# Performance work log

Hardware: AMD Instinct MI355X
Metric: run time of the kernel (lower is better)

Reference implementation:

```python
import jax, jax.numpy as jnp
import numpy as np

D = 512          # latent_dim
H = 8            # num_heads
NLAYERS = 8
DFF = 8          # fast_transformers d_ff slot receives num_heads in the repo (kept faithful)
NC = 10          # NUM_CLUSTERS
KMEANS_ITERS = 10
NJ, NF, T, BS = 25, 6, 1024, 16
NCLS, MAXA = 12, 6


def _pe(S, d):
    pos = jnp.arange(S, dtype=jnp.float32)[:, None]
    div = jnp.exp(jnp.arange(0, d, 2, dtype=jnp.float32) * (-np.log(10000.0) / d))
    pe = jnp.zeros((S, d), jnp.float32)
    pe = pe.at[:, 0::2].set(jnp.sin(pos * div))
    pe = pe.at[:, 1::2].set(jnp.cos(pos * div))
    return pe


def _ln(x, g, b, eps=1e-5):
    m = jnp.mean(x, -1, keepdims=True)
    v = jnp.var(x, -1, keepdims=True)
    return (x - m) * jax.lax.rsqrt(v + eps) * g + b


def _clustered_attn_one(q, k, v):
    # q, k, v: (L, Dh). Cluster queries (Lloyd k-means, deterministic init from
    # first NC queries), attend with centroids, broadcast back to queries.
    cent = q[:NC]
    for _ in range(KMEANS_ITERS):
        d = jnp.sum(cent * cent, -1)[None, :] - 2.0 * (q @ cent.T)  # (L, C)
        a = jnp.argmin(d, -1)
        oh = jax.nn.one_hot(a, NC, dtype=q.dtype)                   # (L, C)
        cent = (oh.T @ q) / jnp.maximum(oh.sum(0), 1.0)[:, None]
    d = jnp.sum(cent * cent, -1)[None, :] - 2.0 * (q @ cent.T)
    a = jnp.argmin(d, -1)                                           # (L,)
    temp = 1.0 / np.sqrt(q.shape[-1])
    A = jax.nn.softmax((cent @ k.T) * temp, -1)                     # (C, L)
    return (A @ v)[a]                                               # (L, Dh)


def _layer(z, Wq, bq, Wk, bk, Wv, bv, Wo, bo, g1, c1, g2, c2, W1, b1, W2, b2):
    B, S, d = z.shape
    Dh = d // H
    q = (z @ Wq + bq).reshape(B, S, H, Dh).transpose(0, 2, 1, 3).reshape(B * H, S, Dh)
    k = (z @ Wk + bk).reshape(B, S, H, Dh).transpose(0, 2, 1, 3).reshape(B * H, S, Dh)
    v = (z @ Wv + bv).reshape(B, S, H, Dh).transpose(0, 2, 1, 3).reshape(B * H, S, Dh)
    o = jax.vmap(_clustered_attn_one)(q, k, v)
    o = o.reshape(B, H, S, Dh).transpose(0, 2, 1, 3).reshape(B, S, d)
    z = z + (o @ Wo + bo)                     # post-norm TransformerEncoderLayer
    z = _ln(z, g1, c1)
    y = jax.nn.relu(z @ W1 + b1) @ W2 + b2    # d_ff == num_heads (repo bug, kept)
    return _ln(z + y, g2, c2)


def _forward(x, muQuery, sigmaQuery, mu_w, mu_b, sig_w, sig_b, skel_w, skel_b,
             Wq, bq, Wk, bk, Wv, bv, Wo, bo, g1, c1, g2, c2, W1, b1, W2, b2, y):
    bs, nj, nf, nframes = x.shape
    h = x.transpose(3, 0, 1, 2).reshape(nframes, bs, nj * nf) @ skel_w + skel_b  # (T,B,D)
    mu_enc = muQuery[y].reshape(bs, -1) @ mu_w + mu_b          # (B, D)
    sig_enc = sigmaQuery[y].reshape(bs, -1) @ sig_w + sig_b    # (B, D)
    xseq = jnp.concatenate([mu_enc[None], sig_enc[None], h], 0)  # (S, B, D)
    S = xseq.shape[0]
    xseq = xseq + _pe(S, xseq.shape[-1])[:, None, :]
    z = xseq.transpose(1, 0, 2)  # (B, S, D): attend over the sequence axis
    for i in range(NLAYERS):
        z = _layer(z, Wq[i], bq[i], Wk[i], bk[i], Wv[i], bv[i], Wo[i], bo[i],
                   g1[i], c1[i], g2[i], c2[i], W1[i], b1[i], W2[i], b2[i])
    out = z.transpose(1, 0, 2)  # (S, B, D)
    return out[0], out[1]       # mu, logvar: (B, D) each


def setup_inputs() -> dict:
    key = jax.random.key(0)
    ks = jax.random.split(key, 20)
    s = 0.02
    return {
        "x": jax.random.normal(ks[0], (BS, NJ, NF, T), jnp.float32),
        "y": jax.random.randint(ks[1], (BS, MAXA), 0, NCLS),
        "mask": jnp.ones((BS, T), bool),
        "muQuery": jax.random.normal(ks[2], (NCLS, D), jnp.float32),
        "sigmaQuery": jax.random.normal(ks[3], (NCLS + 1, D), jnp.float32),
        "mu_w": jax.random.normal(ks[4], (D * MAXA, D), jnp.float32) * s,
        "mu_b": jnp.zeros((D,), jnp.float32),
        "sig_w": jax.random.normal(ks[5], (D * MAXA, D), jnp.float32) * s,
        "sig_b": jnp.zeros((D,), jnp.float32),
        "skel_w": jax.random.normal(ks[6], (NJ * NF, D), jnp.float32) * s,
        "skel_b": jnp.zeros((D,), jnp.float32),
        "Wq": jax.random.normal(ks[7], (NLAYERS, D, D), jnp.float32) * s,
        "bq": jnp.zeros((NLAYERS, D), jnp.float32),
        "Wk": jax.random.normal(ks[8], (NLAYERS, D, D), jnp.float32) * s,
        "bk": jnp.zeros((NLAYERS, D), jnp.float32),
        "Wv": jax.random.normal(ks[9], (NLAYERS, D, D), jnp.float32) * s,
        "bv": jnp.zeros((NLAYERS, D), jnp.float32),
        "Wo": jax.random.normal(ks[10], (NLAYERS, D, D), jnp.float32) * s,
        "bo": jnp.zeros((NLAYERS, D), jnp.float32),
        "g1": jnp.ones((NLAYERS, D), jnp.float32),
        "c1": jnp.zeros((NLAYERS, D), jnp.float32),
        "g2": jnp.ones((NLAYERS, D), jnp.float32),
        "c2": jnp.zeros((NLAYERS, D), jnp.float32),
        "W1": jax.random.normal(ks[11], (NLAYERS, D, DFF), jnp.float32) * s,
        "b1": jnp.zeros((NLAYERS, DFF), jnp.float32),
        "W2": jax.random.normal(ks[12], (NLAYERS, DFF, D), jnp.float32) * s,
        "b2": jnp.zeros((NLAYERS, D), jnp.float32),
    }


def reference(x, y, mask, muQuery, sigmaQuery, mu_w, mu_b, sig_w, sig_b,
              skel_w, skel_b, Wq, bq, Wk, bk, Wv, bv, Wo, bo,
              g1, c1, g2, c2, W1, b1, W2, b2):
    del mask  # computed but never passed to the encoder in the original code
    mu, logvar = _forward(x, muQuery, sigmaQuery, mu_w, mu_b, sig_w, sig_b,
                          skel_w, skel_b, Wq, bq, Wk, bk, Wv, bv, Wo, bo,
                          g1, c1, g2, c2, W1, b1, W2, b2, y)
    return mu, logvar
```

## Files before the change

kernel.cpp:

```cpp
#include <hip/hip_runtime.h>
#include <hip/hip_fp16.h>
#include <math.h>

#define D 512
#define H 8
#define DH 64
#define NLAYERS 8
#define DFF 8
#define NC 10
#define KITERS 10
#define SEQ 1026
#define SEQP 1032
#define BATCH 16
#define MR (BATCH*SEQ)
#define NBUF ((size_t)MR * D)
#define DD ((size_t)D * D)
#define NBH (BATCH*H)

typedef _Float16 f16;
typedef f16 f16x8 __attribute__((ext_vector_type(8)));
typedef float f32x4 __attribute__((ext_vector_type(4)));

__device__ __forceinline__ void split2(float x, float y, unsigned& uh, unsigned& ul) {
    __half hx = __float2half_rn(x), hy = __float2half_rn(y);
    __half lx = __float2half_rn(x - __half2float(hx));
    __half ly = __float2half_rn(y - __half2float(hy));
    uh = (unsigned)__half_as_ushort(hx) | ((unsigned)__half_as_ushort(hy) << 16);
    ul = (unsigned)__half_as_ushort(lx) | ((unsigned)__half_as_ushort(ly) << 16);
}

__device__ __forceinline__ float pe_val(int s, int d) {
    float e = (float)(d & ~1);
    float dv = expf(e * (-9.210340371976184f / 512.0f));
    float ph = (float)s * dv;
    return (d & 1) ? cosf(ph) : sinf(ph);
}

__launch_bounds__(256)
__global__ void convert_w(const float* __restrict__ Wq, const float* __restrict__ Wk,
                          const float* __restrict__ Wv,
                          ushort* __restrict__ whiT, ushort* __restrict__ wloT)
{
    __shared__ float tile[64][65];
    const int tid = threadIdx.x;
    const int k0 = blockIdx.x * 64, n0 = blockIdx.y * 64, m = blockIdx.z;
    const int which = m % 3, lyr = m / 3;
    const float* base;
    switch (which) { case 0: base = Wq; break; case 1: base = Wk; break;
                     default: base = Wv; }
    const float* W = base + (size_t)lyr * DD;
    {
        int r = tid >> 4, c = (tid & 15) * 4;
        #pragma unroll
        for (int p = 0; p < 4; ++p) {
            float4 v = *(const float4*)&W[(size_t)(k0 + r + p*16)*D + n0 + c];
            tile[r + p*16][c]   = v.x; tile[r + p*16][c+1] = v.y;
            tile[r + p*16][c+2] = v.z; tile[r + p*16][c+3] = v.w;
        }
    }
    __syncthreads();
    ushort* ohp = whiT + (size_t)m * DD;
    ushort* olp = wloT + (size_t)m * DD;
    {
        int nl = tid >> 3, kc = (tid & 7) * 8;
        #pragma unroll
        for (int p = 0; p < 2; ++p) {
            int n = nl + p*32;
            uint4 UH, UL;
            split2(tile[kc+0][n], tile[kc+1][n], UH.x, UL.x);
            split2(tile[kc+2][n], tile[kc+3][n], UH.y, UL.y);
            split2(tile[kc+4][n], tile[kc+5][n], UH.z, UL.z);
            split2(tile[kc+6][n], tile[kc+7][n], UH.w, UL.w);
            size_t off = (size_t)(n0 + n)*D + k0 + kc;
            *(uint4*)&ohp[off] = UH;
            *(uint4*)&olp[off] = UL;
        }
    }
}

__launch_bounds__(256)
__global__ void embed_kernel(const float* __restrict__ x, const int* __restrict__ y,
    const float* __restrict__ muQ, const float* __restrict__ sigQ,
    const float* __restrict__ mu_w, const float* __restrict__ mu_b,
    const float* __restrict__ sig_w, const float* __restrict__ sig_b,
    const float* __restrict__ skel_w, const float* __restrict__ skel_b,
    float* __restrict__ z)
{
    __shared__ float xin[3072];
    const int bx = blockIdx.x, b = blockIdx.y, tid = threadIdx.x;
    if (bx < 2) {
        const float* Q  = (bx == 0) ? muQ  : sigQ;
        const float* W  = (bx == 0) ? mu_w : sig_w;
        const float* bb = (bx == 0) ? mu_b : sig_b;
        for (int i = tid; i < 3072; i += 256) {
            int a = y[b*6 + (i >> 9)];
            xin[i] = Q[a*D + (i & 511)];
        }
        __syncthreads();
        const int d0 = tid, d1 = tid + 256;
        float acc0 = bb[d0], acc1 = bb[d1];
        const float4* x4 = (const float4*)xin;
        for (int i4 = 0; i4 < 768; ++i4) {
            float4 xv = x4[i4];
            int r = i4 * 4;
            acc0 += xv.x*W[(size_t)(r+0)*D+d0] + xv.y*W[(size_t)(r+1)*D+d0]
                  + xv.z*W[(size_t)(r+2)*D+d0] + xv.w*W[(size_t)(r+3)*D+d0];
            acc1 += xv.x*W[(size_t)(r+0)*D+d1] + xv.y*W[(size_t)(r+1)*D+d1]
                  + xv.z*W[(size_t)(r+2)*D+d1] + xv.w*W[(size_t)(r+3)*D+d1];
        }
        size_t base = ((size_t)b*SEQ + bx) * D;
        z[base + d0] = acc0 + pe_val(bx, d0);
        z[base + d1] = acc1 + pe_val(bx, d1);
    } else {
        const int f0 = (bx - 2) * 4;
        for (int idx = tid; idx < 600; idx += 256) {
            int i = idx >> 2, ff = idx & 3;
            xin[idx] = x[((size_t)(b*150 + i))*1024 + f0 + ff];
        }
        __syncthreads();
        const float4* x4 = (const float4*)xin;
        for (int dd = 0; dd < 2; ++dd) {
            const int d = tid + dd*256;
            float a0, a1, a2, a3;
            a0 = a1 = a2 = a3 = skel_b[d];
            for (int i = 0; i < 150; ++i) {
                float4 xv = x4[i];
                float w = skel_w[(size_t)i*D + d];
                a0 += xv.x*w; a1 += xv.y*w; a2 += xv.z*w; a3 += xv.w*w;
            }
            float a[4] = {a0, a1, a2, a3};
            #pragma unroll
            for (int ff = 0; ff < 4; ++ff) {
                int s = f0 + ff + 2;
                z[((size_t)b*SEQ + s)*D + d] = a[ff] + pe_val(s, d);
            }
        }
    }
}

__launch_bounds__(256)
__global__ void gemm_qkv(const float* __restrict__ A,
                         const ushort* __restrict__ Bhi_b, const ushort* __restrict__ Blo_b,
                         const float* __restrict__ bq, const float* __restrict__ bk,
                         const float* __restrict__ bv,
                         float* __restrict__ outbase, int M)
{
    __shared__ ushort Ah[128*40], Al[128*40], Bh[128*40], Bl[128*40];
    const int tid = threadIdx.x;
    const int m0 = blockIdx.y * 128, n0 = blockIdx.x * 128;
    const int zz = blockIdx.z;
    const ushort* Bhi = Bhi_b + (size_t)zz * DD;
    const ushort* Blo = Blo_b + (size_t)zz * DD;
    const float* bias = (zz == 0) ? bq : (zz == 1) ? bk : bv;
    float* out = outbase + (size_t)zz * NBUF;
    const int l = tid & 63, wv = tid >> 6;
    const int wr = wv >> 1, wc = wv & 1;

    f32x4 acc[4][4];
    #pragma unroll
    for (int mi = 0; mi < 4; ++mi)
        #pragma unroll
        for (int ni = 0; ni < 4; ++ni) acc[mi][ni] = (f32x4){0.f, 0.f, 0.f, 0.f};

    const int ar_s = tid >> 1, ac_s = (tid & 1) * 16;
    const bool va = (m0 + ar_s) < M;
    const int r0 = (tid*2) >> 2,   kc0 = ((tid*2) & 3) * 8;
    const int r1 = (tid*2+1) >> 2, kc1 = ((tid*2+1) & 3) * 8;
    const float4 fz = make_float4(0.f, 0.f, 0.f, 0.f);

    for (int kt = 0; kt < 16; ++kt) {
        const int kb = kt * 32;
        float4 a0 = fz, a1 = fz, a2 = fz, a3 = fz;
        if (va) {
            const float4* ap = (const float4*)&A[(size_t)(m0 + ar_s)*D + kb + ac_s];
            a0 = ap[0]; a1 = ap[1]; a2 = ap[2]; a3 = ap[3];
        }
        uint4 bh0 = *(const uint4*)&Bhi[(size_t)(n0+r0)*D + kb + kc0];
        uint4 bh1 = *(const uint4*)&Bhi[(size_t)(n0+r1)*D + kb + kc1];
        uint4 bl0 = *(const uint4*)&Blo[(size_t)(n0+r0)*D + kb + kc0];
        uint4 bl1 = *(const uint4*)&Blo[(size_t)(n0+r1)*D + kb + kc1];

        uint4 AH0, AL0, AH1, AL1;
        split2(a0.x, a0.y, AH0.x, AL0.x); split2(a0.z, a0.w, AH0.y, AL0.y);
        split2(a1.x, a1.y, AH0.z, AL0.z); split2(a1.z, a1.w, AH0.w, AL0.w);
        split2(a2.x, a2.y, AH1.x, AL1.x); split2(a2.z, a2.w, AH1.y, AL1.y);
        split2(a3.x, a3.y, AH1.z, AL1.z); split2(a3.z, a3.w, AH1.w, AL1.w);

        if (kt) __syncthreads();
        *(uint4*)&Ah[ar_s*40 + ac_s]     = AH0;
        *(uint4*)&Ah[ar_s*40 + ac_s + 8] = AH1;
        *(uint4*)&Al[ar_s*40 + ac_s]     = AL0;
        *(uint4*)&Al[ar_s*40 + ac_s + 8] = AL1;
        *(uint4*)&Bh[r0*40 + kc0] = bh0;  *(uint4*)&Bh[r1*40 + kc1] = bh1;
        *(uint4*)&Bl[r0*40 + kc0] = bl0;  *(uint4*)&Bl[r1*40 + kc1] = bl1;
        __syncthreads();

        const int ko = (l >> 4) * 8;
        f16x8 bhf[4], blf[4];
        #pragma unroll
        for (int ni = 0; ni < 4; ++ni) {
            int br = wc*64 + ni*16 + (l & 15);
            bhf[ni] = *(const f16x8*)&Bh[br*40 + ko];
            blf[ni] = *(const f16x8*)&Bl[br*40 + ko];
        }
        #pragma unroll
        for (int mi = 0; mi < 4; ++mi) {
            int ar = wr*64 + mi*16 + (l & 15);
            f16x8 ahf = *(const f16x8*)&Ah[ar*40 + ko];
            f16x8 alf = *(const f16x8*)&Al[ar*40 + ko];
            #pragma unroll
            for (int ni = 0; ni < 4; ++ni) {
                acc[mi][ni] = __builtin_amdgcn_mfma_f32_16x16x32_f16(ahf, bhf[ni], acc[mi][ni], 0, 0, 0);
                acc[mi][ni] = __builtin_amdgcn_mfma_f32_16x16x32_f16(ahf, blf[ni], acc[mi][ni], 0, 0, 0);
                acc[mi][ni] = __builtin_amdgcn_mfma_f32_16x16x32_f16(alf, bhf[ni], acc[mi][ni], 0, 0, 0);
            }
        }
    }

    const int col_base = n0 + wc*64 + (l & 15);
    const int row_base = m0 + wr*64 + ((l >> 4) << 2);
    #pragma unroll
    for (int ni = 0; ni < 4; ++ni) {
        const int col = col_base + ni*16;
        const float bv2 = bias[col];
        #pragma unroll
        for (int mi = 0; mi < 4; ++mi) {
            #pragma unroll
            for (int e = 0; e < 4; ++e) {
                const int row = row_base + mi*16 + e;
                if (row >= M) continue;
                float val = acc[mi][ni][e] + bv2;
                int bb = row / SEQ;
                int ss = row - bb*SEQ;
                int hh = col >> 6, dh = col & 63;
                out[((size_t)(bb*H + hh)*SEQ + ss)*DH + dh] = val;
            }
        }
    }
}

__launch_bounds__(1024, 4)
__global__ void attn_kernel(const float* __restrict__ q, const float* __restrict__ kk,
                            const float* __restrict__ v,
                            float* __restrict__ centout, unsigned char* __restrict__ assignout)
{
    __shared__ float At[NC][SEQP];
    __shared__ float cent[NC][DH];
    __shared__ float tailrow[2][DH];
    __shared__ float cnorm[NC];
    __shared__ int   cnt[NC];
    __shared__ int   chg;
    __shared__ unsigned char assign[1028];
    __shared__ float redA[16][NC];
    __shared__ float redB[16][NC];
    __shared__ float Mc[NC];
    __shared__ float Sinv[NC];

    const int tid = threadIdx.x;
    const int wv = tid >> 6, lane = tid & 63;
    const int bh = blockIdx.x;
    const float* qh = q  + (size_t)bh * SEQ * DH;
    const float* kh = kk + (size_t)bh * SEQ * DH;
    const float* vh = v  + (size_t)bh * SEQ * DH;
    float* part = &At[0][0];

    if (tid < NC*DH) ((float*)cent)[tid] = qh[tid];
    if (tid >= NC*DH && tid < NC*DH + 2*DH) ((float*)tailrow)[tid - NC*DH] = qh[1024*DH + (tid - NC*DH)];
    __syncthreads();

    const float4* qrow4 = (const float4*)(qh + (size_t)tid * DH);
    int prev_a = -1, prev_t = -1;

    for (int iter = 0; iter <= KITERS; ++iter) {
        if (tid < NC) {
            float sn = 0.f;
            #pragma unroll
            for (int i = 0; i < 16; ++i) {
                float4 cv = *(const float4*)&cent[tid][i*4];
                sn += cv.x*cv.x + cv.y*cv.y + cv.z*cv.z + cv.w*cv.w;
            }
            cnorm[tid] = sn;
            cnt[tid] = 0;
        }
        if (tid == 0) chg = 0;
        __syncthreads();

        int a_reg;
        {
            float acc[NC];
            #pragma unroll
            for (int c = 0; c < NC; ++c) acc[c] = 0.f;
            #pragma unroll 8
            for (int kq = 0; kq < 16; ++kq) {
                float4 qv = qrow4[kq];
                #pragma unroll
                for (int c = 0; c < NC; ++c) {
                    float4 cv = *(const float4*)&cent[c][kq*4];
                    acc[c] += qv.x*cv.x + qv.y*cv.y + qv.z*cv.z + qv.w*cv.w;
                }
            }
            int best = 0; float bd = 1e30f;
            #pragma unroll
            for (int c = 0; c < NC; ++c) {
                float dd = cnorm[c] - 2.f*acc[c];
                if (dd < bd) { bd = dd; best = c; }
            }
            a_reg = best;
            assign[tid] = (unsigned char)best;
        }
        {
            unsigned long long mm = __ballot(a_reg != prev_a);
            if (lane == 0 && mm) atomicAdd(&chg, 1);
            prev_a = a_reg;
        }
        if (iter < KITERS) {
            #pragma unroll
            for (int c = 0; c < NC; ++c) {
                unsigned long long m = __ballot(a_reg == c);
                if (lane == 0 && m) atomicAdd(&cnt[c], __popcll(m));
            }
        }
        if (tid < 2) {
            int best = 0; float bd = 1e30f;
            #pragma unroll
            for (int c = 0; c < NC; ++c) {
                float acc = 0.f;
                #pragma unroll
                for (int i = 0; i < 64; ++i) acc += tailrow[tid][i]*cent[c][i];
                float dd = cnorm[c] - 2.f*acc;
                if (dd < bd) { bd = dd; best = c; }
            }
            assign[1024 + tid] = (unsigned char)best;
            if (best != prev_t) atomicAdd(&chg, 1);
            prev_t = best;
            if (iter < KITERS) atomicAdd(&cnt[best], 1);
        }
        __syncthreads();
        if (iter == KITERS) break;
        if (chg == 0) break;

        {
            float accq[NC];
            #pragma unroll
            for (int c = 0; c < NC; ++c) accq[c] = 0.f;
            const int s0 = wv * 64;
            #pragma unroll 8
            for (int i = 0; i < 64; ++i) {
                int s = s0 + i;
                float qv = qh[(size_t)s*DH + lane];
                int c = assign[s];
                #pragma unroll
                for (int cc = 0; cc < NC; ++cc) accq[cc] += (cc == c) ? qv : 0.f;
            }
            if (wv < 2) {
                int c = assign[1024 + wv];
                float qv = tailrow[wv][lane];
                #pragma unroll
                for (int cc = 0; cc < NC; ++cc) accq[cc] += (cc == c) ? qv : 0.f;
            }
            #pragma unroll
            for (int c = 0; c < NC; ++c) part[(wv*NC + c)*DH + lane] = accq[c];
        }
        __syncthreads();
        if (tid < NC*DH) {
            int c = tid >> 6;
            float s = 0.f;
            #pragma unroll
            for (int w = 0; w < 16; ++w) s += part[w*(NC*DH) + tid];
            ((float*)cent)[tid] = s / fmaxf((float)cnt[c], 1.f);
        }
        __syncthreads();
    }

    if (tid < 2*DH) ((float*)tailrow)[tid] = kh[1024*DH + tid];
    __syncthreads();

    float lg[NC], lgt[NC];
    {
        const float4* krow4 = (const float4*)(kh + (size_t)tid * DH);
        #pragma unroll
        for (int c = 0; c < NC; ++c) lg[c] = 0.f;
        #pragma unroll 8
        for (int kq = 0; kq < 16; ++kq) {
            float4 kv = krow4[kq];
            #pragma unroll
            for (int c = 0; c < NC; ++c) {
                float4 cv = *(const float4*)&cent[c][kq*4];
                lg[c] += kv.x*cv.x + kv.y*cv.y + kv.z*cv.z + kv.w*cv.w;
            }
        }
        #pragma unroll
        for (int c = 0; c < NC; ++c) lg[c] *= 0.125f;
    }
    if (tid < 2) {
        #pragma unroll
        for (int c = 0; c < NC; ++c) {
            float acc = 0.f;
            #pragma unroll
            for (int i = 0; i < 64; ++i) acc += tailrow[tid][i]*cent[c][i];
            lgt[c] = 0.125f * acc;
        }
    }

    #pragma unroll
    for (int c = 0; c < NC; ++c) {
        float m = lg[c];
        if (tid < 2) m = fmaxf(m, lgt[c]);
        #pragma unroll
        for (int off = 32; off; off >>= 1) m = fmaxf(m, __shfl_xor(m, off, 64));
        if (lane == 0) redA[wv][c] = m;
    }
    __syncthreads();
    if (tid < NC) {
        float m = redA[0][tid];
        #pragma unroll
        for (int w = 1; w < 16; ++w) m = fmaxf(m, redA[w][tid]);
        Mc[tid] = m;
    }
    __syncthreads();
    #pragma unroll
    for (int c = 0; c < NC; ++c) lg[c] = expf(lg[c] - Mc[c]);
    if (tid < 2) {
        #pragma unroll
        for (int c = 0; c < NC; ++c) lgt[c] = expf(lgt[c] - Mc[c]);
    }
    #pragma unroll
    for (int c = 0; c < NC; ++c) {
        float s = lg[c] + ((tid < 2) ? lgt[c] : 0.f);
        #pragma unroll
        for (int off = 32; off; off >>= 1) s += __shfl_xor(s, off, 64);
        if (lane == 0) redB[wv][c] = s;
    }
    __syncthreads();
    if (tid < NC) {
        float s = 0.f;
        #pragma unroll
        for (int w = 0; w < 16; ++w) s += redB[w][tid];
        Sinv[tid] = 1.f / s;
    }
    __syncthreads();
    #pragma unroll
    for (int c = 0; c < NC; ++c) At[c][tid] = lg[c] * Sinv[c];
    if (tid < 2) {
        #pragma unroll
        for (int c = 0; c < NC; ++c) At[c][1024 + tid] = lgt[c] * Sinv[c];
    }
    __syncthreads();

    {
        float accv[NC];
        #pragma unroll
        for (int c = 0; c < NC; ++c) accv[c] = 0.f;
        const int s0 = wv * 64;
        for (int i = 0; i < 64; i += 4) {
            float vv0 = vh[(size_t)(s0+i  )*DH + lane];
            float vv1 = vh[(size_t)(s0+i+1)*DH + lane];
            float vv2 = vh[(size_t)(s0+i+2)*DH + lane];
            float vv3 = vh[(size_t)(s0+i+3)*DH + lane];
            #pragma unroll
            for (int c = 0; c < NC; ++c) {
                float4 av = *(const float4*)&At[c][s0+i];
                accv[c] += av.x*vv0 + av.y*vv1 + av.z*vv2 + av.w*vv3;
            }
        }
        if (wv < 2) {
            int s = 1024 + wv;
            float vv = vh[(size_t)s*DH + lane];
            #pragma unroll
            for (int c = 0; c < NC; ++c) accv[c] += At[c][s] * vv;
        }
        __syncthreads();
        #pragma unroll
        for (int c = 0; c < NC; ++c) part[(wv*NC + c)*DH + lane] = accv[c];
    }
    __syncthreads();
    if (tid < NC*DH) {
        float s = 0.f;
        #pragma unroll
        for (int w = 0; w < 16; ++w) s += part[w*(NC*DH) + tid];
        centout[(size_t)bh*(NC*DH) + tid] = s;
    }
    for (int i = tid; i < SEQ; i += 1024)
        assignout[(size_t)bh*SEQP + i] = assign[i];
}

__launch_bounds__(256)
__global__ void pproj_kernel(const float* __restrict__ centout, const float* __restrict__ Wo,
                             float* __restrict__ P)
{
    __shared__ float cs[NC][DH];
    const int tid = threadIdx.x;
    const int bh = blockIdx.x, h = bh & 7;
    const int n = blockIdx.y * 256 + tid;
    for (int i = tid; i < NC*DH; i += 256) ((float*)cs)[i] = centout[(size_t)bh*(NC*DH) + i];
    __syncthreads();
    float acc[NC];
    #pragma unroll
    for (int c = 0; c < NC; ++c) acc[c] = 0.f;
    #pragma unroll 8
    for (int d = 0; d < DH; ++d) {
        float wv = Wo[(size_t)(h*DH + d)*D + n];
        #pragma unroll
        for (int c = 0; c < NC; ++c) acc[c] += cs[c][d] * wv;
    }
    #pragma unroll
    for (int c = 0; c < NC; ++c)
        P[((size_t)bh*NC + c)*D + n] = acc[c];
}

__launch_bounds__(256)
__global__ void ffn_ln_kernel(float* __restrict__ z,
    const float* __restrict__ P, const unsigned char* __restrict__ assignbuf,
    const float* __restrict__ bo,
    const float* __restrict__ g1, const float* __restrict__ c1,
    const float* __restrict__ W1, const float* __restrict__ b1,
    const float* __restrict__ W2, const float* __restrict__ b2,
    const float* __restrict__ g2, const float* __restrict__ c2)
{
    __shared__ float red[8];
    __shared__ float redh[4][DFF];
    const int row = blockIdx.x, tid = threadIdx.x;
    const int lane = tid & 63, wid = tid >> 6;
    const int b = row / SEQ, s = row - b*SEQ;

    float x0 = z[(size_t)row*D + tid]       + bo[tid];
    float x1 = z[(size_t)row*D + tid + 256] + bo[tid + 256];
    #pragma unroll
    for (int h = 0; h < H; ++h) {
        int a = assignbuf[(size_t)(b*H + h)*SEQP + s];
        const float* Pr = P + ((size_t)(b*H + h)*NC + a)*D;
        x0 += Pr[tid];
        x1 += Pr[tid + 256];
    }

    float sm = x0 + x1, ss = x0*x0 + x1*x1;
    #pragma unroll
    for (int off = 32; off; off >>= 1) {
        sm += __shfl_xor(sm, off, 64);
        ss += __shfl_xor(ss, off, 64);
    }
    if (lane == 0) { red[wid] = sm; red[4 + wid] = ss; }
    __syncthreads();
    float tot  = red[0] + red[1] + red[2] + red[3];
    float tot2 = red[4] + red[5] + red[6] + red[7];
    float mean = tot * (1.f/512.f);
    float var  = tot2 * (1.f/512.f) - mean*mean;
    float rstd = rsqrtf(var + 1e-5f);
    float za = (x0 - mean)*rstd*g1[tid]       + c1[tid];
    float zb = (x1 - mean)*rstd*g1[tid + 256] + c1[tid + 256];

    float p[DFF];
    #pragma unroll
    for (int j = 0; j < DFF; ++j)
        p[j] = za * W1[(size_t)tid*DFF + j] + zb * W1[(size_t)(tid+256)*DFF + j];
    #pragma unroll
    for (int off = 32; off; off >>= 1)
        #pragma unroll
        for (int j = 0; j < DFF; ++j) p[j] += __shfl_xor(p[j], off, 64);
    if (lane == 0) {
        #pragma unroll
        for (int j = 0; j < DFF; ++j) redh[wid][j] = p[j];
    }
    __syncthreads();
    float hv[DFF];
    #pragma unroll
    for (int j = 0; j < DFF; ++j)
        hv[j] = fmaxf(redh[0][j] + redh[1][j] + redh[2][j] + redh[3][j] + b1[j], 0.f);
    float y0 = b2[tid], y1 = b2[tid + 256];
    #pragma unroll
    for (int j = 0; j < DFF; ++j) {
        y0 += hv[j] * W2[(size_t)j*D + tid];
        y1 += hv[j] * W2[(size_t)j*D + tid + 256];
    }
    float t0 = za + y0, t1 = zb + y1;
    float s2 = t0 + t1, ss2 = t0*t0 + t1*t1;
    #pragma unroll
    for (int off = 32; off; off >>= 1) {
        s2  += __shfl_xor(s2,  off, 64);
        ss2 += __shfl_xor(ss2, off, 64);
    }
    if (lane == 0) { red[wid] = s2; red[4 + wid] = ss2; }
    __syncthreads();
    float tt  = red[0] + red[1] + red[2] + red[3];
    float tt2 = red[4] + red[5] + red[6] + red[7];
    float m2 = tt * (1.f/512.f);
    float v2 = tt2 * (1.f/512.f) - m2*m2;
    float rstd2 = rsqrtf(v2 + 1e-5f);
    float* zo = z + (size_t)row * D;
    zo[tid]       = (t0 - m2)*rstd2*g2[tid]       + c2[tid];
    zo[tid + 256] = (t1 - m2)*rstd2*g2[tid + 256] + c2[tid + 256];
}

__launch_bounds__(256)
__global__ void extract_kernel(const float* __restrict__ z, float* __restrict__ out) {
    int i = blockIdx.x * 256 + threadIdx.x;
    if (i >= 2*BATCH*D) return;
    int half = i >> 13;
    int j = i & 8191;
    int b = j >> 9, d = j & 511;
    out[i] = z[((size_t)b*SEQ + half)*D + d];
}

extern "C" void kernel_launch(void* const* d_in, const int* in_sizes, int n_in,
                              void* d_out, int out_size, void* d_ws, size_t ws_size,
                              hipStream_t stream)
{
    const float* x      = (const float*)d_in[0];
    const int*   y      = (const int*)  d_in[1];
    const float* muQ    = (const float*)d_in[3];
    const float* sigQ   = (const float*)d_in[4];
    const float* mu_w   = (const float*)d_in[5];
    const float* mu_b   = (const float*)d_in[6];
    const float* sig_w  = (const float*)d_in[7];
    const float* sig_b  = (const float*)d_in[8];
    const float* skel_w = (const float*)d_in[9];
    const float* skel_b = (const float*)d_in[10];
    const float* Wq     = (const float*)d_in[11];
    const float* bq     = (const float*)d_in[12];
    const float* Wk     = (const float*)d_in[13];
    const float* bk     = (const float*)d_in[14];
    const float* Wv     = (const float*)d_in[15];
    const float* bv     = (const float*)d_in[16];
    const float* Wo     = (const float*)d_in[17];
    const float* bo     = (const float*)d_in[18];
    const float* g1     = (const float*)d_in[19];
    const float* c1     = (const float*)d_in[20];
    const float* g2     = (const float*)d_in[21];
    const float* c2     = (const float*)d_in[22];
    const float* W1     = (const float*)d_in[23];
    const float* b1     = (const float*)d_in[24];
    const float* W2     = (const float*)d_in[25];
    const float* b2     = (const float*)d_in[26];

    float*  z    = (float*)d_ws;
    float*  qb   = z  + NBUF;
    float*  kb   = qb + NBUF;
    float*  vb   = kb + NBUF;
    ushort* wThi = (ushort*)(vb + NBUF);
    ushort* wTlo = wThi + 24*DD;
    float*  centbuf = (float*)(wTlo + 24*DD);
    float*  P       = centbuf + (size_t)NBH*NC*DH;
    unsigned char* assignbuf = (unsigned char*)(P + (size_t)NBH*NC*D);

    convert_w<<<dim3(8, 8, 24), 256, 0, stream>>>(Wq, Wk, Wv, wThi, wTlo);

    embed_kernel<<<dim3(258, BATCH), 256, 0, stream>>>(
        x, y, muQ, sigQ, mu_w, mu_b, sig_w, sig_b, skel_w, skel_b, z);

    for (int l = 0; l < NLAYERS; ++l) {
        gemm_qkv<<<dim3(4, 129, 3), 256, 0, stream>>>(
            z, wThi + (size_t)l*3*DD, wTlo + (size_t)l*3*DD,
            bq + l*D, bk + l*D, bv + l*D, qb, MR);
        attn_kernel<<<NBH, 1024, 0, stream>>>(qb, kb, vb, centbuf, assignbuf);
        pproj_kernel<<<dim3(NBH, 2), 256, 0, stream>>>(centbuf, Wo + (size_t)l*DD, P);
        ffn_ln_kernel<<<MR, 256, 0, stream>>>(z, P, assignbuf, bo + l*D,
            g1 + (size_t)l*D, c1 + (size_t)l*D,
            W1 + (size_t)l*D*DFF, b1 + (size_t)l*DFF,
            W2 + (size_t)l*DFF*D, b2 + (size_t)l*D,
            g2 + (size_t)l*D, c2 + (size_t)l*D);
    }
    extract_kernel<<<64, 256, 0, stream>>>(z, (float*)d_out);

    (void)in_sizes; (void)n_in; (void)out_size; (void)ws_size;
}
```

Before: 4.468 ms.

## Split k-means clustering into multi-block assign/update kernels across sequence chunks

Replaces the single-block-per-head k-means loop inside the attention kernel with separate assign and update kernels launched over 5 sequence chunks per head. Partial centroid sums and counts go to global memory and are reduced at the start of the next assign launch, and the final attention kernel only computes centroid attention. This raises parallelism from 128 blocks to 640 blocks during clustering. In exchange it adds about 21 extra kernel launches per layer and drops the early-exit on convergence, so all iterations always run.

```diff
diff --git a/kernel.cpp b/kernel.cpp
--- a/kernel.cpp
+++ b/kernel.cpp
@@ -16,6 +16,7 @@
 #define NBUF ((size_t)MR * D)
 #define DD ((size_t)D * D)
 #define NBH (BATCH*H)
+#define NCHUNK 5
 
 typedef _Float16 f16;
 typedef f16 f16x8 __attribute__((ext_vector_type(8)));
@@ -239,18 +240,129 @@
     }
 }
 
+template<bool INIT>
+__launch_bounds__(256)
+__global__ void kassign(const float* __restrict__ q,
+                        const float* __restrict__ partials, const float* __restrict__ pcnt,
+                        unsigned char* __restrict__ assignbuf)
+{
+    __shared__ float cent[NC][DH];
+    __shared__ float cnorm[NC];
+    __shared__ float cntS[NC];
+    const int tid = threadIdx.x;
+    const int chunk = blockIdx.x, head = blockIdx.y;
+    const float* qh = q + (size_t)head * SEQ * DH;
+
+    if (INIT) {
+        for (int i = tid; i < NC*DH; i += 256) ((float*)cent)[i] = qh[i];
+    } else {
+        if (tid < NC) {
+            float s = 0.f;
+            #pragma unroll
+            for (int j = 0; j < NCHUNK; ++j) s += pcnt[((size_t)head*NCHUNK + j)*NC + tid];
+            cntS[tid] = fmaxf(s, 1.f);
+        }
+        __syncthreads();
+        for (int i = tid; i < NC*DH; i += 256) {
+            int c = i >> 6;
+            float s = 0.f;
+            #pragma unroll
+            for (int j = 0; j < NCHUNK; ++j) s += partials[((size_t)head*NCHUNK + j)*(NC*DH) + i];
+            ((float*)cent)[i] = s / cntS[c];
+        }
+    }
+    __syncthreads();
+    if (tid < NC) {
+        float sn = 0.f;
+        #pragma unroll
+        for (int i = 0; i < 16; ++i) {
+            float4 cv = *(const float4*)&cent[tid][i*4];
+            sn += cv.x*cv.x + cv.y*cv.y + cv.z*cv.z + cv.w*cv.w;
+        }
+        cnorm[tid] = sn;
+    }
+    __syncthreads();
+
+    const int s = chunk*256 + tid;
+    if (s < SEQ) {
+        const float4* qrow4 = (const float4*)(qh + (size_t)s * DH);
+        float acc[NC];
+        #pragma unroll
+        for (int c = 0; c < NC; ++c) acc[c] = 0.f;
+        #pragma unroll 8
+        for (int kq = 0; kq < 16; ++kq) {
+            float4 qv = qrow4[kq];
+            #pragma unroll
+            for (int c = 0; c < NC; ++c) {
+                float4 cv = *(const float4*)&cent[c][kq*4];
+                acc[c] += qv.x*cv.x + qv.y*cv.y + qv.z*cv.z + qv.w*cv.w;
+            }
+        }
+        int best = 0; float bd = 1e30f;
+        #pragma unroll
+        for (int c = 0; c < NC; ++c) {
+            float dd = cnorm[c] - 2.f*acc[c];
+            if (dd < bd) { bd = dd; best = c; }
+        }
+        assignbuf[(size_t)head*SEQP + s] = (unsigned char)best;
+    }
+}
+
+__launch_bounds__(256)
+__global__ void kupdate(const float* __restrict__ q,
+                        const unsigned char* __restrict__ assignbuf,
+                        float* __restrict__ partials, float* __restrict__ pcnt)
+{
+    __shared__ float part[4][NC][DH];
+    __shared__ float pcw[4][NC];
+    const int tid = threadIdx.x;
+    const int wv = tid >> 6, lane = tid & 63;
+    const int chunk = blockIdx.x, head = blockIdx.y;
+    const float* qh = q + (size_t)head * SEQ * DH;
+    const unsigned char* ah = assignbuf + (size_t)head * SEQP;
+
+    float accq[NC], cw[NC];
+    #pragma unroll
+    for (int c = 0; c < NC; ++c) { accq[c] = 0.f; cw[c] = 0.f; }
+    const int s0 = chunk*256 + wv*64;
+    #pragma unroll 8
+    for (int i = 0; i < 64; ++i) {
+        int s = s0 + i;
+        if (s < SEQ) {
+            float qv = qh[(size_t)s*DH + lane];
+            int c = ah[s];
+            #pragma unroll
+            for (int cc = 0; cc < NC; ++cc) {
+                accq[cc] += (cc == c) ? qv : 0.f;
+                cw[cc]   += (cc == c) ? 1.f : 0.f;
+            }
+        }
+    }
+    #pragma unroll
+    for (int c = 0; c < NC; ++c) part[wv][c][lane] = accq[c];
+    if (lane == 0) {
+        #pragma unroll
+        for (int c = 0; c < NC; ++c) pcw[wv][c] = cw[c];
+    }
+    __syncthreads();
+    float* pp = partials + ((size_t)head*NCHUNK + chunk)*(NC*DH);
+    for (int i = tid; i < NC*DH; i += 256) {
+        const float* pf = &part[0][0][0];
+        pp[i] = pf[i] + pf[640 + i] + pf[1280 + i] + pf[1920 + i];
+    }
+    if (tid < NC)
+        pcnt[((size_t)head*NCHUNK + chunk)*NC + tid] = pcw[0][tid] + pcw[1][tid] + pcw[2][tid] + pcw[3][tid];
+}
+
 __launch_bounds__(1024, 4)
-__global__ void attn_kernel(const float* __restrict__ q, const float* __restrict__ kk,
-                            const float* __restrict__ v,
-                            float* __restrict__ centout, unsigned char* __restrict__ assignout)
+__global__ void attn_final(const float* __restrict__ kk, const float* __restrict__ v,
+                           const float* __restrict__ partials, const float* __restrict__ pcnt,
+                           float* __restrict__ centout)
 {
     __shared__ float At[NC][SEQP];
     __shared__ float cent[NC][DH];
     __shared__ float tailrow[2][DH];
-    __shared__ float cnorm[NC];
-    __shared__ int   cnt[NC];
-    __shared__ int   chg;
-    __shared__ unsigned char assign[1028];
+    __shared__ float cntS[NC];
     __shared__ float redA[16][NC];
     __shared__ float redB[16][NC];
     __shared__ float Mc[NC];
@@ -259,120 +371,25 @@
     const int tid = threadIdx.x;
     const int wv = tid >> 6, lane = tid & 63;
     const int bh = blockIdx.x;
-    const float* qh = q  + (size_t)bh * SEQ * DH;
     const float* kh = kk + (size_t)bh * SEQ * DH;
     const float* vh = v  + (size_t)bh * SEQ * DH;
     float* part = &At[0][0];
 
-    if (tid < NC*DH) ((float*)cent)[tid] = qh[tid];
-    if (tid >= NC*DH && tid < NC*DH + 2*DH) ((float*)tailrow)[tid - NC*DH] = qh[1024*DH + (tid - NC*DH)];
-    __syncthreads();
-
-    const float4* qrow4 = (const float4*)(qh + (size_t)tid * DH);
-    int prev_a = -1, prev_t = -1;
-
-    for (int iter = 0; iter <= KITERS; ++iter) {
-        if (tid < NC) {
-            float sn = 0.f;
-            #pragma unroll
-            for (int i = 0; i < 16; ++i) {
-                float4 cv = *(const float4*)&cent[tid][i*4];
-                sn += cv.x*cv.x + cv.y*cv.y + cv.z*cv.z + cv.w*cv.w;
-            }
-            cnorm[tid] = sn;
-            cnt[tid] = 0;
-        }
-        if (tid == 0) chg = 0;
-        __syncthreads();
-
-        int a_reg;
-        {
-            float acc[NC];
-            #pragma unroll
-            for (int c = 0; c < NC; ++c) acc[c] = 0.f;
-            #pragma unroll 8
-            for (int kq = 0; kq < 16; ++kq) {
-                float4 qv = qrow4[kq];
-                #pragma unroll
-                for (int c = 0; c < NC; ++c) {
-                    float4 cv = *(const float4*)&cent[c][kq*4];
-                    acc[c] += qv.x*cv.x + qv.y*cv.y + qv.z*cv.z + qv.w*cv.w;
-                }
-            }
-            int best = 0; float bd = 1e30f;
-            #pragma unroll
-            for (int c = 0; c < NC; ++c) {
-                float dd = cnorm[c] - 2.f*acc[c];
-                if (dd < bd) { bd = dd; best = c; }
-            }
-            a_reg = best;
-            assign[tid] = (unsigned char)best;
-        }
-        {
-            unsigned long long mm = __ballot(a_reg != prev_a);
-            if (lane == 0 && mm) atomicAdd(&chg, 1);
-            prev_a = a_reg;
-        }
-        if (iter < KITERS) {
-            #pragma unroll
-            for (int c = 0; c < NC; ++c) {
-                unsigned long long m = __ballot(a_reg == c);
-                if (lane == 0 && m) atomicAdd(&cnt[c], __popcll(m));
-            }
-        }
-        if (tid < 2) {
-            int best = 0; float bd = 1e30f;
-            #pragma unroll
-            for (int c = 0; c < NC; ++c) {
-                float acc = 0.f;
-                #pragma unroll
-                for (int i = 0; i < 64; ++i) acc += tailrow[tid][i]*cent[c][i];
-                float dd = cnorm[c] - 2.f*acc;
-                if (dd < bd) { bd = dd; best = c; }
-            }
-            assign[1024 + tid] = (unsigned char)best;
-            if (best != prev_t) atomicAdd(&chg, 1);
-            prev_t = best;
-            if (iter < KITERS) atomicAdd(&cnt[best], 1);
-        }
-        __syncthreads();
-        if (iter == KITERS) break;
-        if (chg == 0) break;
-
-        {
-            float accq[NC];
-            #pragma unroll
-            for (int c = 0; c < NC; ++c) accq[c] = 0.f;
-            const int s0 = wv * 64;
-            #pragma unroll 8
-            for (int i = 0; i < 64; ++i) {
-                int s = s0 + i;
-                float qv = qh[(size_t)s*DH + lane];
-                int c = assign[s];
-                #pragma unroll
-                for (int cc = 0; cc < NC; ++cc) accq[cc] += (cc == c) ? qv : 0.f;
-            }
-            if (wv < 2) {
-                int c = assign[1024 + wv];
-                float qv = tailrow[wv][lane];
-                #pragma unroll
-                for (int cc = 0; cc < NC; ++cc) accq[cc] += (cc == c) ? qv : 0.f;
-            }
-            #pragma unroll
-            for (int c = 0; c < NC; ++c) part[(wv*NC + c)*DH + lane] = accq[c];
-        }
-        __syncthreads();
-        if (tid < NC*DH) {
-            int c = tid >> 6;
-            float s = 0.f;
-            #pragma unroll
-            for (int w = 0; w < 16; ++w) s += part[w*(NC*DH) + tid];
-            ((float*)cent)[tid] = s / fmaxf((float)cnt[c], 1.f);
-        }
-        __syncthreads();
-    }
-
-    if (tid < 2*DH) ((float*)tailrow)[tid] = kh[1024*DH + tid];
+    if (tid < NC) {
+        float s = 0.f;
+        #pragma unroll
+        for (int j = 0; j < NCHUNK; ++j) s += pcnt[((size_t)bh*NCHUNK + j)*NC + tid];
+        cntS[tid] = fmaxf(s, 1.f);
+    }
+    __syncthreads();
+    if (tid < NC*DH) {
+        int c = tid >> 6;
+        float s = 0.f;
+        #pragma unroll
+        for (int j = 0; j < NCHUNK; ++j) s += partials[((size_t)bh*NCHUNK + j)*(NC*DH) + tid];
+        ((float*)cent)[tid] = s / cntS[c];
+    }
+    if (tid >= NC*DH && tid < NC*DH + 2*DH) ((float*)tailrow)[tid - NC*DH] = kh[1024*DH + (tid - NC*DH)];
     __syncthreads();
 
     float lg[NC], lgt[NC];
@@ -480,8 +497,6 @@
         for (int w = 0; w < 16; ++w) s += part[w*(NC*DH) + tid];
         centout[(size_t)bh*(NC*DH) + tid] = s;
     }
-    for (int i = tid; i < SEQ; i += 1024)
-        assignout[(size_t)bh*SEQP + i] = assign[i];
 }
 
 __launch_bounds__(256)
@@ -638,8 +653,10 @@
     float*  vb   = kb + NBUF;
     ushort* wThi = (ushort*)(vb + NBUF);
     ushort* wTlo = wThi + 24*DD;
-    float*  centbuf = (float*)(wTlo + 24*DD);
-    float*  P       = centbuf + (size_t)NBH*NC*DH;
+    float*  partials = (float*)(wTlo + 24*DD);
+    float*  pcnt     = partials + (size_t)NBH*NCHUNK*NC*DH;
+    float*  centbuf  = pcnt + (size_t)NBH*NCHUNK*NC;
+    float*  P        = centbuf + (size_t)NBH*NC*DH;
     unsigned char* assignbuf = (unsigned char*)(P + (size_t)NBH*NC*D);
 
     convert_w<<<dim3(8, 8, 24), 256, 0, stream>>>(Wq, Wk, Wv, wThi, wTlo);
@@ -651,7 +668,12 @@
         gemm_qkv<<<dim3(4, 129, 3), 256, 0, stream>>>(
             z, wThi + (size_t)l*3*DD, wTlo + (size_t)l*3*DD,
             bq + l*D, bk + l*D, bv + l*D, qb, MR);
-        attn_kernel<<<NBH, 1024, 0, stream>>>(qb, kb, vb, centbuf, assignbuf);
+        kassign<true><<<dim3(NCHUNK, NBH), 256, 0, stream>>>(qb, partials, pcnt, assignbuf);
+        for (int it = 0; it < KITERS; ++it) {
+            kupdate<<<dim3(NCHUNK, NBH), 256, 0, stream>>>(qb, assignbuf, partials, pcnt);
+            kassign<false><<<dim3(NCHUNK, NBH), 256, 0, stream>>>(qb, partials, pcnt, assignbuf);
+        }
+        attn_final<<<NBH, 1024, 0, stream>>>(kb, vb, partials, pcnt, centbuf);
         pproj_kernel<<<dim3(NBH, 2), 256, 0, stream>>>(centbuf, Wo + (size_t)l*DD, P);
         ffn_ln_kernel<<<MR, 256, 0, stream>>>(z, P, assignbuf, bo + l*D,
             g1 + (size_t)l*D, c1 + (size_t)l*D,
```

After: 5.258 ms. 1.18x slower.

## Store Q transposed per head for coalesced k-means reads in attention

Applied to the files above, without the earlier changes.

The QKV GEMM now writes Q in a per-head transposed layout (DH x SEQP), so the k-means distance loop reads Q coalesced across threads. Previously each thread read its own row with strided float4 loads. The centroid update is reorganised so each wave owns four dimensions and reduces over sequence positions with wavefront shuffles, replacing the shared-memory partial sums and the 16-way reduction. The price is scattered, uncoalesced stores of Q in the GEMM epilogue and an extra shared array.

```diff
diff --git a/kernel.cpp b/kernel.cpp
--- a/kernel.cpp
+++ b/kernel.cpp
@@ -16,6 +16,7 @@
 #define NBUF ((size_t)MR * D)
 #define DD ((size_t)D * D)
 #define NBH (BATCH*H)
+#define QTSZ ((size_t)NBH * DH * SEQP)
 
 typedef _Float16 f16;
 typedef f16 f16x8 __attribute__((ext_vector_type(8)));
@@ -143,7 +144,8 @@
                          const ushort* __restrict__ Bhi_b, const ushort* __restrict__ Blo_b,
                          const float* __restrict__ bq, const float* __restrict__ bk,
                          const float* __restrict__ bv,
-                         float* __restrict__ outbase, int M)
+                         float* __restrict__ qoutT, float* __restrict__ kout,
+                         float* __restrict__ vout, int M)
 {
     __shared__ ushort Ah[128*40], Al[128*40], Bh[128*40], Bl[128*40];
     const int tid = threadIdx.x;
@@ -152,7 +154,7 @@
     const ushort* Bhi = Bhi_b + (size_t)zz * DD;
     const ushort* Blo = Blo_b + (size_t)zz * DD;
     const float* bias = (zz == 0) ? bq : (zz == 1) ? bk : bv;
-    float* out = outbase + (size_t)zz * NBUF;
+    float* out = (zz == 0) ? qoutT : (zz == 1) ? kout : vout;
     const int l = tid & 63, wv = tid >> 6;
     const int wr = wv >> 1, wc = wv & 1;
 
@@ -223,6 +225,7 @@
     for (int ni = 0; ni < 4; ++ni) {
         const int col = col_base + ni*16;
         const float bv2 = bias[col];
+        const int hh = col >> 6, dh = col & 63;
         #pragma unroll
         for (int mi = 0; mi < 4; ++mi) {
             #pragma unroll
@@ -232,20 +235,24 @@
                 float val = acc[mi][ni][e] + bv2;
                 int bb = row / SEQ;
                 int ss = row - bb*SEQ;
-                int hh = col >> 6, dh = col & 63;
-                out[((size_t)(bb*H + hh)*SEQ + ss)*DH + dh] = val;
+                if (zz == 0) {
+                    out[((size_t)(bb*H + hh)*DH + dh)*SEQP + ss] = val;
+                } else {
+                    out[((size_t)(bb*H + hh)*SEQ + ss)*DH + dh] = val;
+                }
             }
         }
     }
 }
 
 __launch_bounds__(1024, 4)
-__global__ void attn_kernel(const float* __restrict__ q, const float* __restrict__ kk,
+__global__ void attn_kernel(const float* __restrict__ qT, const float* __restrict__ kk,
                             const float* __restrict__ v,
                             float* __restrict__ centout, unsigned char* __restrict__ assignout)
 {
     __shared__ float At[NC][SEQP];
     __shared__ float cent[NC][DH];
+    __shared__ float centN[NC][DH];
     __shared__ float tailrow[2][DH];
     __shared__ float cnorm[NC];
     __shared__ int   cnt[NC];
@@ -259,18 +266,22 @@
     const int tid = threadIdx.x;
     const int wv = tid >> 6, lane = tid & 63;
     const int bh = blockIdx.x;
-    const float* qh = q  + (size_t)bh * SEQ * DH;
+    const float* qh = qT + (size_t)bh * DH * SEQP;
     const float* kh = kk + (size_t)bh * SEQ * DH;
     const float* vh = v  + (size_t)bh * SEQ * DH;
     float* part = &At[0][0];
 
-    if (tid < NC*DH) ((float*)cent)[tid] = qh[tid];
-    if (tid >= NC*DH && tid < NC*DH + 2*DH) ((float*)tailrow)[tid - NC*DH] = qh[1024*DH + (tid - NC*DH)];
-    __syncthreads();
-
-    const float4* qrow4 = (const float4*)(qh + (size_t)tid * DH);
+    if (tid < NC*DH) {
+        int c = tid >> 6, d = tid & 63;
+        cent[c][d] = qh[(size_t)d*SEQP + c];
+    }
+    if (tid >= NC*DH && tid < NC*DH + 2*DH) {
+        int i = tid - NC*DH, t = i >> 6, d = i & 63;
+        tailrow[t][d] = qh[(size_t)d*SEQP + 1024 + t];
+    }
+    __syncthreads();
+
     int prev_a = -1, prev_t = -1;
-
     for (int iter = 0; iter <= KITERS; ++iter) {
         if (tid < NC) {
             float sn = 0.f;
@@ -290,13 +301,16 @@
             float acc[NC];
             #pragma unroll
             for (int c = 0; c < NC; ++c) acc[c] = 0.f;
-            #pragma unroll 8
-            for (int kq = 0; kq < 16; ++kq) {
-                float4 qv = qrow4[kq];
+            #pragma unroll 4
+            for (int d4 = 0; d4 < 16; ++d4) {
+                float q0 = qh[(size_t)(d4*4+0)*SEQP + tid];
+                float q1 = qh[(size_t)(d4*4+1)*SEQP + tid];
+                float q2 = qh[(size_t)(d4*4+2)*SEQP + tid];
+                float q3 = qh[(size_t)(d4*4+3)*SEQP + tid];
                 #pragma unroll
                 for (int c = 0; c < NC; ++c) {
-                    float4 cv = *(const float4*)&cent[c][kq*4];
-                    acc[c] += qv.x*cv.x + qv.y*cv.y + qv.z*cv.z + qv.w*cv.w;
+                    float4 cv = *(const float4*)&cent[c][d4*4];
+                    acc[c] += q0*cv.x + q1*cv.y + q2*cv.z + q3*cv.w;
                 }
             }
             int best = 0; float bd = 1e30f;
@@ -340,34 +354,39 @@
         if (chg == 0) break;
 
         {
-            float accq[NC];
-            #pragma unroll
-            for (int c = 0; c < NC; ++c) accq[c] = 0.f;
-            const int s0 = wv * 64;
-            #pragma unroll 8
-            for (int i = 0; i < 64; ++i) {
-                int s = s0 + i;
-                float qv = qh[(size_t)s*DH + lane];
-                int c = assign[s];
+            #pragma unroll
+            for (int dd = 0; dd < 4; ++dd) {
+                const int d = wv*4 + dd;
+                float accq[NC];
                 #pragma unroll
-                for (int cc = 0; cc < NC; ++cc) accq[cc] += (cc == c) ? qv : 0.f;
-            }
-            if (wv < 2) {
-                int c = assign[1024 + wv];
-                float qv = tailrow[wv][lane];
+                for (int c = 0; c < NC; ++c) accq[c] = 0.f;
+                #pragma unroll 4
+                for (int i = 0; i < 16; ++i) {
+                    int s = i*64 + lane;
+                    float qv = qh[(size_t)d*SEQP + s];
+                    int c = assign[s];
+                    #pragma unroll
+                    for (int cc = 0; cc < NC; ++cc) accq[cc] += (cc == c) ? qv : 0.f;
+                }
+                if (lane < 2) {
+                    int c = assign[1024 + lane];
+                    float qv = tailrow[lane][d];
+                    #pragma unroll
+                    for (int cc = 0; cc < NC; ++cc) accq[cc] += (cc == c) ? qv : 0.f;
+                }
                 #pragma unroll
-                for (int cc = 0; cc < NC; ++cc) accq[cc] += (cc == c) ? qv : 0.f;
-            }
-            #pragma unroll
-            for (int c = 0; c < NC; ++c) part[(wv*NC + c)*DH + lane] = accq[c];
+                for (int c = 0; c < NC; ++c) {
+                    float s = accq[c];
+                    #pragma unroll
+                    for (int off = 32; off; off >>= 1) s += __shfl_xor(s, off, 64);
+                    if (lane == 0) centN[c][d] = s;
+                }
+            }
         }
         __syncthreads();
         if (tid < NC*DH) {
-            int c = tid >> 6;
-            float s = 0.f;
-            #pragma unroll
-            for (int w = 0; w < 16; ++w) s += part[w*(NC*DH) + tid];
-            ((float*)cent)[tid] = s / fmaxf((float)cnt[c], 1.f);
+            int c = tid >> 6, d = tid & 63;
+            cent[c][d] = centN[c][d] / fmaxf((float)cnt[c], 1.f);
         }
         __syncthreads();
     }
@@ -634,12 +653,12 @@
 
     float*  z    = (float*)d_ws;
     float*  qb   = z  + NBUF;
-    float*  kb   = qb + NBUF;
+    float*  kb   = qb + QTSZ;
     float*  vb   = kb + NBUF;
     ushort* wThi = (ushort*)(vb + NBUF);
     ushort* wTlo = wThi + 24*DD;
-    float*  centbuf = (float*)(wTlo + 24*DD);
-    float*  P       = centbuf + (size_t)NBH*NC*DH;
+    float*  centbuf  = (float*)(wTlo + 24*DD);
+    float*  P        = centbuf + (size_t)NBH*NC*DH;
     unsigned char* assignbuf = (unsigned char*)(P + (size_t)NBH*NC*D);
 
     convert_w<<<dim3(8, 8, 24), 256, 0, stream>>>(Wq, Wk, Wv, wThi, wTlo);
@@ -650,7 +669,7 @@
     for (int l = 0; l < NLAYERS; ++l) {
         gemm_qkv<<<dim3(4, 129, 3), 256, 0, stream>>>(
             z, wThi + (size_t)l*3*DD, wTlo + (size_t)l*3*DD,
-            bq + l*D, bk + l*D, bv + l*D, qb, MR);
+            bq + l*D, bk + l*D, bv + l*D, qb, kb, vb, MR);
         attn_kernel<<<NBH, 1024, 0, stream>>>(qb, kb, vb, centbuf, assignbuf);
         pproj_kernel<<<dim3(NBH, 2), 256, 0, stream>>>(centbuf, Wo + (size_t)l*DD, P);
         ffn_ln_kernel<<<MR, 256, 0, stream>>>(z, P, assignbuf, bo + l*D,
```

New measurement: 5.256 ms. 1.18x slower.
